# Kernel optimization log

Hardware: AMD Instinct MI355X
Metric: run time of the kernel (lower is better)

The kernel has to match this reference:

```python
import jax, jax.numpy as jnp
import numpy as np

EMBED_DIM = 1024
NUM_HEADS = 16
HEAD_DIM = EMBED_DIM // NUM_HEADS
B, S = 4, 2048


def setup_inputs() -> dict:
    key = jax.random.key(0)
    ks = jax.random.split(key, 9)
    scale = 1.0 / np.sqrt(EMBED_DIM)
    x = jax.random.normal(ks[0], (B, S, EMBED_DIM), dtype=jnp.float32)
    Wq = jax.random.normal(ks[1], (EMBED_DIM, EMBED_DIM), dtype=jnp.float32) * scale
    Wk = jax.random.normal(ks[2], (EMBED_DIM, EMBED_DIM), dtype=jnp.float32) * scale
    Wv = jax.random.normal(ks[3], (EMBED_DIM, EMBED_DIM), dtype=jnp.float32) * scale
    Wo = jax.random.normal(ks[4], (EMBED_DIM, EMBED_DIM), dtype=jnp.float32) * scale
    bq = jnp.zeros((EMBED_DIM,), jnp.float32)
    bk = jnp.zeros((EMBED_DIM,), jnp.float32)
    bv = jnp.zeros((EMBED_DIM,), jnp.float32)
    bo = jnp.zeros((EMBED_DIM,), jnp.float32)
    return {"x": x, "Wq": Wq, "bq": bq, "Wk": Wk, "bk": bk, "Wv": Wv, "bv": bv, "Wo": Wo, "bo": bo}


def _split_heads(t):
    # [B,S,E] -> [B,H,S,D]
    b, s, _ = t.shape
    return t.reshape(b, s, NUM_HEADS, HEAD_DIM).transpose(0, 2, 1, 3)


def reference(x, Wq, bq, Wk, bk, Wv, bv, Wo, bo):
    q = _split_heads(x @ Wq + bq)
    k = _split_heads(x @ Wk + bk)
    v = _split_heads(x @ Wv + bv)
    scale = 1.0 / jnp.sqrt(jnp.asarray(HEAD_DIM, x.dtype))
    scores = jnp.einsum('bhqd,bhkd->bhqk', q, k) * scale  # [B,H,S,S]
    weights = jax.nn.softmax(scores, axis=-1)
    attn = jnp.einsum('bhqk,bhkd->bhqd', weights, v)  # [B,H,S,D]
    b, h, s, d = attn.shape
    concat = attn.transpose(0, 2, 1, 3).reshape(b, s, h * d)
    return concat @ Wo + bo
```

## Files before the change

### kernel.cpp

```cpp
#include <hip/hip_runtime.h>
#include <hip/hip_bf16.h>

typedef unsigned short u16;
typedef __attribute__((ext_vector_type(8))) short bf16x8;
typedef __attribute__((ext_vector_type(4))) float f32x4;
typedef __attribute__((ext_vector_type(4))) unsigned short u16x4;

#define EMB 1024
#define SEQ 2048
#define NH 16
#define HD 64

#define OFF_WT   0u
#define OFF_WOT  3145728u
#define OFF_Q    4194304u
#define OFF_K    12582912u
#define OFF_VT   20971520u
#define OFF_OC   29360128u

#define QSCALE 0.1803368801111f

__device__ __forceinline__ u16 f2bf(float f) {
    unsigned int x; __builtin_memcpy(&x, &f, 4);
    unsigned int r = x + 0x7fffu + ((x >> 16) & 1u);
    return (u16)(r >> 16);
}

#if defined(__has_builtin) && __has_builtin(__builtin_amdgcn_cvt_pk_bf16_f32)
typedef __attribute__((ext_vector_type(2))) __bf16 bfv2;
__device__ __forceinline__ unsigned int pkbf(float a, float b) {
    bfv2 v = __builtin_amdgcn_cvt_pk_bf16_f32(a, b);
    unsigned int u; __builtin_memcpy(&u, &v, 4); return u;
}
#else
__device__ __forceinline__ unsigned int pkbf(float a, float b) {
    return (unsigned)f2bf(a) | ((unsigned)f2bf(b) << 16);
}
#endif

#if defined(__has_builtin) && __has_builtin(__builtin_amdgcn_exp2f)
__device__ __forceinline__ float exp2fast(float x) { return __builtin_amdgcn_exp2f(x); }
#else
__device__ __forceinline__ float exp2fast(float x) { return __builtin_exp2f(x); }
#endif

__device__ __forceinline__ void gld_lds16(const void* gsrc, void* ldst) {
    void* g = const_cast<void*>(gsrc);
    __builtin_amdgcn_global_load_lds((__attribute__((address_space(1))) void*)g,
                                     (__attribute__((address_space(3))) void*)ldst,
                                     16, 0, 0);
}

__global__ __launch_bounds__(256) void convert_x(
    const float* __restrict__ x, u16* __restrict__ xb)
{
    int i = (blockIdx.x * 256 + threadIdx.x) * 4;
    float4 v = *(const float4*)&x[i];
    uint2 o = { pkbf(v.x, v.y), pkbf(v.z, v.w) };
    *(uint2*)&xb[i] = o;
}

__global__ __launch_bounds__(256) void transpose_w(
    const float* __restrict__ W0, const float* __restrict__ W1,
    const float* __restrict__ W2, const float* __restrict__ W3,
    u16* __restrict__ ws)
{
    __shared__ u16 tile[64 * 65];
    const float* src = blockIdx.z == 0 ? W0 : blockIdx.z == 1 ? W1 : blockIdx.z == 2 ? W2 : W3;
    u16* dst = ws + (blockIdx.z < 3 ? (unsigned)blockIdx.z * 1048576u : OFF_WOT);
    const int k0 = blockIdx.x * 64, n0 = blockIdx.y * 64;
    const int t = threadIdx.x;
    #pragma unroll
    for (int i = 0; i < 16; i++) {
        int idx = i * 256 + t; int r = idx >> 6, c = idx & 63;
        tile[c * 65 + r] = f2bf(src[(k0 + r) * EMB + n0 + c]);
    }
    __syncthreads();
    #pragma unroll
    for (int i = 0; i < 16; i++) {
        int idx = i * 256 + t; int r = idx >> 6, c = idx & 63;
        dst[(n0 + r) * EMB + k0 + c] = tile[r * 65 + c];
    }
}

__global__ __launch_bounds__(256) void gemm_qkv(
    const u16* __restrict__ X, const u16* __restrict__ WT,
    const float* __restrict__ bq, const float* __restrict__ bk, const float* __restrict__ bv,
    u16* __restrict__ Qt, u16* __restrict__ Ko, u16* __restrict__ Vt)
{
    __shared__ u16 Al[128 * 32];
    __shared__ u16 Bl[128 * 32];
    const int t = threadIdx.x, lane = t & 63, w = t >> 6;
    const int quad = lane >> 4, l15 = lane & 15;
    const int wr = w >> 1, wc = w & 1;
    const int m0 = blockIdx.x * 128, n0 = blockIdx.y * 128;
    const f32x4 fzero = {0.f, 0.f, 0.f, 0.f};

    f32x4 acc[4][4];
    #pragma unroll
    for (int i = 0; i < 4; i++)
        #pragma unroll
        for (int j = 0; j < 4; j++) acc[i][j] = fzero;

    for (int kt = 0; kt < 32; ++kt) {
        #pragma unroll
        for (int r = 0; r < 2; r++) {
            int g = r * 256 + t; int row = g >> 2, cw = g & 3;
            int sc = (cw ^ ((row >> 1) & 3)) * 8;
            gld_lds16(X  + (size_t)(m0 + row) * EMB + kt * 32 + sc, &Al[g * 8]);
            gld_lds16(WT + (size_t)(n0 + row) * EMB + kt * 32 + sc, &Bl[g * 8]);
        }
        __syncthreads();
        bf16x8 af[4], bfr[4];
        #pragma unroll
        for (int i = 0; i < 4; i++) {
            int rowA = wr * 64 + i * 16 + l15;
            af[i] = *(const bf16x8*)&Al[rowA * 32 + ((quad ^ ((rowA >> 1) & 3)) * 8)];
        }
        #pragma unroll
        for (int j = 0; j < 4; j++) {
            int rowB = wc * 64 + j * 16 + l15;
            bfr[j] = *(const bf16x8*)&Bl[rowB * 32 + ((quad ^ ((rowB >> 1) & 3)) * 8)];
        }
        #pragma unroll
        for (int i = 0; i < 4; i++)
            #pragma unroll
            for (int j = 0; j < 4; j++)
                acc[i][j] = __builtin_amdgcn_mfma_f32_16x16x32_bf16(af[i], bfr[j], acc[i][j], 0, 0, 0);
        __syncthreads();
    }

    const int seg = n0 >> 10;
    const float* bias = seg == 0 ? bq : (seg == 1 ? bk : bv);
    #pragma unroll
    for (int j = 0; j < 4; j++) {
        int n = n0 + wc * 64 + j * 16 + l15;
        int nn = n & 1023;
        float bvl = bias[nn];
        int h = nn >> 6, d = nn & 63;
        #pragma unroll
        for (int i = 0; i < 4; i++) {
            int m = m0 + wr * 64 + i * 16 + quad * 4;
            int b = m >> 11, s = m & 2047;
            if (seg == 0) {
                uint2 pp = { pkbf((acc[i][j][0] + bvl) * QSCALE, (acc[i][j][1] + bvl) * QSCALE),
                             pkbf((acc[i][j][2] + bvl) * QSCALE, (acc[i][j][3] + bvl) * QSCALE) };
                *(uint2*)&Qt[(size_t)((b * NH + h) * HD + d) * SEQ + s] = pp;
            } else if (seg == 2) {
                uint2 pp = { pkbf(acc[i][j][0] + bvl, acc[i][j][1] + bvl),
                             pkbf(acc[i][j][2] + bvl, acc[i][j][3] + bvl) };
                *(uint2*)&Vt[(size_t)((b * NH + h) * HD + d) * SEQ + s] = pp;
            } else {
                size_t base = (size_t)((b * NH + h) * SEQ + s) * HD + d;
                #pragma unroll
                for (int r = 0; r < 4; r++) Ko[base + (size_t)r * HD] = f2bf(acc[i][j][r] + bvl);
            }
        }
    }
}

__global__ __launch_bounds__(256, 2) void flash_attn(
    const u16* __restrict__ Q, const u16* __restrict__ K,
    const u16* __restrict__ VT, u16* __restrict__ Oc)
{
    __shared__ u16 Kl[2][64 * 64];
    __shared__ u16 Vl[2][64 * 64];
    __shared__ u16 Pl[4][2][16 * 72];
    const int t = threadIdx.x, lane = t & 63, w = t >> 6;
    const int quad = lane >> 4, l15 = lane & 15;
    const int a7 = l15 & 7;
    const int bh = blockIdx.y;
    const int b = bh >> 4, h = bh & 15;
    const int q0 = blockIdx.x * 256 + w * 64;
    const u16* Qtb = Q + (size_t)bh * HD * SEQ;
    const u16* Kb  = K + (size_t)bh * SEQ * HD;
    const u16* Vb  = VT + (size_t)bh * HD * SEQ;
    const f32x4 fzero = {0.f, 0.f, 0.f, 0.f};

    const int kf0 = l15 * 64 + ((quad ^ a7) * 8);
    const int kf1 = l15 * 64 + (((4 + quad) ^ a7) * 8);
    u16* pww = &Pl[w][0][l15 * 72 + quad * 4];
    const u16* pwr = &Pl[w][0][l15 * 72 + quad * 8];

    bf16x8 ones;
    #pragma unroll
    for (int j = 0; j < 8; j++) ones[j] = (short)0x3F80;

    bf16x8 qf[4][2];
    #pragma unroll
    for (int i = 0; i < 4; i++)
        #pragma unroll
        for (int c = 0; c < 2; c++)
            #pragma unroll
            for (int j = 0; j < 8; j++)
                qf[i][c][j] = (short)Qtb[(size_t)(c * 32 + quad * 8 + j) * SEQ + q0 + i * 16 + l15];

    f32x4 oacc[4][4];
    f32x4 oextra[4];
    #pragma unroll
    for (int i = 0; i < 4; i++) {
        oextra[i] = fzero;
        #pragma unroll
        for (int f = 0; f < 4; f++) oacc[i][f] = fzero;
    }

    auto stage = [&](int kt, int bsel) {
        #pragma unroll
        for (int r = 0; r < 2; r++) {
            int g = r * 256 + t, row = g >> 3, cw = g & 7;
            int swz = (cw ^ (row & 7)) * 8;
            gld_lds16(Kb + (size_t)kt * 64 * HD + row * HD + swz, &Kl[bsel][g * 8]);
            gld_lds16(Vb + (size_t)row * SEQ + kt * 64 + swz, &Vl[bsel][g * 8]);
        }
    };

    stage(0, 0);
    asm volatile("s_waitcnt vmcnt(0) lgkmcnt(0)" ::: "memory");
    __builtin_amdgcn_s_barrier();
    __builtin_amdgcn_sched_barrier(0);

    int cur = 0;
    for (int kt = 0; kt < 32; ++kt) {
        if (kt < 31) stage(kt + 1, cur ^ 1);

        const u16* kbuf = &Kl[cur][0];
        const u16* vbuf = &Vl[cur][0];
        bf16x8 ak[2][4], av[2][4];
        #pragma unroll
        for (int f = 0; f < 4; f++) {
            ak[0][f] = *(const bf16x8*)(kbuf + kf0 + f * 1024);
            ak[1][f] = *(const bf16x8*)(kbuf + kf1 + f * 1024);
            av[0][f] = *(const bf16x8*)(vbuf + kf0 + f * 1024);
            av[1][f] = *(const bf16x8*)(vbuf + kf1 + f * 1024);
        }

        #pragma unroll
        for (int i = 0; i < 4; i++) {
            const int par = (i & 1) * 1152;
            f32x4 sf[4];
            #pragma unroll
            for (int f = 0; f < 4; f++) sf[f] = fzero;
            __builtin_amdgcn_s_setprio(1);
            #pragma unroll
            for (int c = 0; c < 2; c++)
                #pragma unroll
                for (int f = 0; f < 4; f++)
                    sf[f] = __builtin_amdgcn_mfma_f32_16x16x32_bf16(ak[c][f], qf[i][c], sf[f], 0, 0, 0);
            __builtin_amdgcn_s_setprio(0);

            #pragma unroll
            for (int f = 0; f < 4; f++) {
                float p0 = exp2fast(sf[f][0]);
                float p1 = exp2fast(sf[f][1]);
                float p2 = exp2fast(sf[f][2]);
                float p3 = exp2fast(sf[f][3]);
                uint2 pp = { pkbf(p0, p1), pkbf(p2, p3) };
                *(uint2*)(pww + par + f * 16) = pp;
            }
            bf16x8 bp0 = *(const bf16x8*)(pwr + par);
            bf16x8 bp1 = *(const bf16x8*)(pwr + par + 32);

            __builtin_amdgcn_s_setprio(1);
            #pragma unroll
            for (int f = 0; f < 4; f++) {
                oacc[i][f] = __builtin_amdgcn_mfma_f32_16x16x32_bf16(av[0][f], bp0, oacc[i][f], 0, 0, 0);
                oacc[i][f] = __builtin_amdgcn_mfma_f32_16x16x32_bf16(av[1][f], bp1, oacc[i][f], 0, 0, 0);
            }
            oextra[i] = __builtin_amdgcn_mfma_f32_16x16x32_bf16(ones, bp0, oextra[i], 0, 0, 0);
            oextra[i] = __builtin_amdgcn_mfma_f32_16x16x32_bf16(ones, bp1, oextra[i], 0, 0, 0);
            __builtin_amdgcn_s_setprio(0);
        }

        if (kt < 31) {
            asm volatile("s_waitcnt vmcnt(0) lgkmcnt(0)" ::: "memory");
            __builtin_amdgcn_s_barrier();
            __builtin_amdgcn_sched_barrier(0);
        }
        cur ^= 1;
    }

    #pragma unroll
    for (int i = 0; i < 4; i++) {
        float inv = 1.0f / oextra[i][0];
        int s = q0 + i * 16 + l15;
        size_t base = ((size_t)(b * SEQ + s) * NH + h) * HD;
        #pragma unroll
        for (int f = 0; f < 4; f++) {
            uint2 o = { pkbf(oacc[i][f][0] * inv, oacc[i][f][1] * inv),
                        pkbf(oacc[i][f][2] * inv, oacc[i][f][3] * inv) };
            *(uint2*)&Oc[base + f * 16 + quad * 4] = o;
        }
    }
}

__global__ __launch_bounds__(256) void gemm_out(
    const u16* __restrict__ A, const u16* __restrict__ WT,
    const float* __restrict__ bo, float* __restrict__ out)
{
    __shared__ u16 Al[128 * 32];
    __shared__ u16 Bl[128 * 32];
    const int t = threadIdx.x, lane = t & 63, w = t >> 6;
    const int quad = lane >> 4, l15 = lane & 15;
    const int wr = w >> 1, wc = w & 1;
    const int m0 = blockIdx.x * 128, n0 = blockIdx.y * 128;
    const f32x4 fzero = {0.f, 0.f, 0.f, 0.f};

    f32x4 acc[4][4];
    #pragma unroll
    for (int i = 0; i < 4; i++)
        #pragma unroll
        for (int j = 0; j < 4; j++) acc[i][j] = fzero;

    for (int kt = 0; kt < 32; ++kt) {
        #pragma unroll
        for (int r = 0; r < 2; r++) {
            int g = r * 256 + t; int row = g >> 2, cw = g & 3;
            int sc = (cw ^ ((row >> 1) & 3)) * 8;
            gld_lds16(A  + (size_t)(m0 + row) * EMB + kt * 32 + sc, &Al[g * 8]);
            gld_lds16(WT + (size_t)(n0 + row) * EMB + kt * 32 + sc, &Bl[g * 8]);
        }
        __syncthreads();
        bf16x8 af[4], bfr[4];
        #pragma unroll
        for (int i = 0; i < 4; i++) {
            int rowA = wr * 64 + i * 16 + l15;
            af[i] = *(const bf16x8*)&Al[rowA * 32 + ((quad ^ ((rowA >> 1) & 3)) * 8)];
        }
        #pragma unroll
        for (int j = 0; j < 4; j++) {
            int rowB = wc * 64 + j * 16 + l15;
            bfr[j] = *(const bf16x8*)&Bl[rowB * 32 + ((quad ^ ((rowB >> 1) & 3)) * 8)];
        }
        #pragma unroll
        for (int i = 0; i < 4; i++)
            #pragma unroll
            for (int j = 0; j < 4; j++)
                acc[i][j] = __builtin_amdgcn_mfma_f32_16x16x32_bf16(af[i], bfr[j], acc[i][j], 0, 0, 0);
        __syncthreads();
    }

    #pragma unroll
    for (int j = 0; j < 4; j++) {
        int n = n0 + wc * 64 + j * 16 + l15;
        float bvl = bo[n];
        #pragma unroll
        for (int i = 0; i < 4; i++) {
            int m = m0 + wr * 64 + i * 16 + quad * 4;
            #pragma unroll
            for (int r = 0; r < 4; r++)
                out[(size_t)(m + r) * EMB + n] = acc[i][j][r] + bvl;
        }
    }
}

extern "C" void kernel_launch(void* const* d_in, const int* in_sizes, int n_in,
                              void* d_out, int out_size, void* d_ws, size_t ws_size,
                              hipStream_t stream)
{
    (void)in_sizes; (void)n_in; (void)out_size; (void)ws_size;
    const float* x  = (const float*)d_in[0];
    const float* Wq = (const float*)d_in[1];
    const float* bq = (const float*)d_in[2];
    const float* Wk = (const float*)d_in[3];
    const float* bk = (const float*)d_in[4];
    const float* Wv = (const float*)d_in[5];
    const float* bv = (const float*)d_in[6];
    const float* Wo = (const float*)d_in[7];
    const float* bo = (const float*)d_in[8];
    u16* ws = (u16*)d_ws;
    u16* Xb = (u16*)d_out;

    convert_x<<<dim3(8192), 256, 0, stream>>>(x, Xb);
    transpose_w<<<dim3(16, 16, 4), 256, 0, stream>>>(Wq, Wk, Wv, Wo, ws);
    gemm_qkv<<<dim3(64, 24), 256, 0, stream>>>(Xb, ws + OFF_WT, bq, bk, bv,
                                               ws + OFF_Q, ws + OFF_K, ws + OFF_VT);
    flash_attn<<<dim3(8, 64), 256, 0, stream>>>(ws + OFF_Q, ws + OFF_K,
                                                ws + OFF_VT, ws + OFF_OC);
    gemm_out<<<dim3(64, 8), 256, 0, stream>>>(ws + OFF_OC, ws + OFF_WOT, bo, (float*)d_out);
}
```

Before: 295.9 us.

## Replace LDS round-trip for P with permlane swaps and remap blocks per XCD

The softmax probabilities P are no longer written to shared memory and read back in the B-operand layout. They are rearranged between lanes in registers using v_permlane32_swap and v_permlane16_swap, which removes the LDS traffic and the per-wave P buffer. Separately, the launch becomes a 1D grid that is remapped so that all query tiles of a given (batch, head) land on the same XCD, which should improve L2 reuse of K and V. The risk is that the permlane shuffle pattern must exactly reproduce the old LDS layout transform, or the results will be wrong.

```diff
diff --git a/kernel.cpp b/kernel.cpp
--- a/kernel.cpp
+++ b/kernel.cpp
@@ -4,7 +4,7 @@
 typedef unsigned short u16;
 typedef __attribute__((ext_vector_type(8))) short bf16x8;
 typedef __attribute__((ext_vector_type(4))) float f32x4;
-typedef __attribute__((ext_vector_type(4))) unsigned short u16x4;
+typedef __attribute__((ext_vector_type(4))) unsigned int u32x4;
 
 #define EMB 1024
 #define SEQ 2048
@@ -165,13 +165,17 @@
 {
     __shared__ u16 Kl[2][64 * 64];
     __shared__ u16 Vl[2][64 * 64];
-    __shared__ u16 Pl[4][2][16 * 72];
     const int t = threadIdx.x, lane = t & 63, w = t >> 6;
     const int quad = lane >> 4, l15 = lane & 15;
     const int a7 = l15 & 7;
-    const int bh = blockIdx.y;
+
+    const int lin = blockIdx.x;
+    const int xcd = lin & 7, slot = lin >> 3;
+    const int bh = xcd * 8 + (slot >> 3);
+    const int qx = slot & 7;
     const int b = bh >> 4, h = bh & 15;
-    const int q0 = blockIdx.x * 256 + w * 64;
+    const int q0 = qx * 256 + w * 64;
+
     const u16* Qtb = Q + (size_t)bh * HD * SEQ;
     const u16* Kb  = K + (size_t)bh * SEQ * HD;
     const u16* Vb  = VT + (size_t)bh * HD * SEQ;
@@ -179,8 +183,6 @@
 
     const int kf0 = l15 * 64 + ((quad ^ a7) * 8);
     const int kf1 = l15 * 64 + (((4 + quad) ^ a7) * 8);
-    u16* pww = &Pl[w][0][l15 * 72 + quad * 4];
-    const u16* pwr = &Pl[w][0][l15 * 72 + quad * 8];
 
     bf16x8 ones;
     #pragma unroll
@@ -236,7 +238,6 @@
 
         #pragma unroll
         for (int i = 0; i < 4; i++) {
-            const int par = (i & 1) * 1152;
             f32x4 sf[4];
             #pragma unroll
             for (int f = 0; f < 4; f++) sf[f] = fzero;
@@ -248,17 +249,29 @@
                     sf[f] = __builtin_amdgcn_mfma_f32_16x16x32_bf16(ak[c][f], qf[i][c], sf[f], 0, 0, 0);
             __builtin_amdgcn_s_setprio(0);
 
+            unsigned int pa[4][2];
             #pragma unroll
             for (int f = 0; f < 4; f++) {
-                float p0 = exp2fast(sf[f][0]);
-                float p1 = exp2fast(sf[f][1]);
-                float p2 = exp2fast(sf[f][2]);
-                float p3 = exp2fast(sf[f][3]);
-                uint2 pp = { pkbf(p0, p1), pkbf(p2, p3) };
-                *(uint2*)(pww + par + f * 16) = pp;
+                pa[f][0] = pkbf(exp2fast(sf[f][0]), exp2fast(sf[f][1]));
+                pa[f][1] = pkbf(exp2fast(sf[f][2]), exp2fast(sf[f][3]));
             }
-            bf16x8 bp0 = *(const bf16x8*)(pwr + par);
-            bf16x8 bp1 = *(const bf16x8*)(pwr + par + 32);
+
+            unsigned int z0 = pa[0][0], w0 = pa[1][0];
+            asm("v_permlane32_swap_b32 %0, %1" : "+v"(z0), "+v"(w0));
+            asm("v_permlane16_swap_b32 %0, %1" : "+v"(z0), "+v"(w0));
+            unsigned int z1 = pa[0][1], w1 = pa[1][1];
+            asm("v_permlane32_swap_b32 %0, %1" : "+v"(z1), "+v"(w1));
+            asm("v_permlane16_swap_b32 %0, %1" : "+v"(z1), "+v"(w1));
+            unsigned int z2 = pa[2][0], w2 = pa[3][0];
+            asm("v_permlane32_swap_b32 %0, %1" : "+v"(z2), "+v"(w2));
+            asm("v_permlane16_swap_b32 %0, %1" : "+v"(z2), "+v"(w2));
+            unsigned int z3 = pa[2][1], w3 = pa[3][1];
+            asm("v_permlane32_swap_b32 %0, %1" : "+v"(z3), "+v"(w3));
+            asm("v_permlane16_swap_b32 %0, %1" : "+v"(z3), "+v"(w3));
+
+            bf16x8 bp0, bp1;
+            { u32x4 u = {z0, z1, w0, w1}; __builtin_memcpy(&bp0, &u, 16); }
+            { u32x4 u = {z2, z3, w2, w3}; __builtin_memcpy(&bp1, &u, 16); }
 
             __builtin_amdgcn_s_setprio(1);
             #pragma unroll
@@ -374,7 +387,7 @@
     transpose_w<<<dim3(16, 16, 4), 256, 0, stream>>>(Wq, Wk, Wv, Wo, ws);
     gemm_qkv<<<dim3(64, 24), 256, 0, stream>>>(Xb, ws + OFF_WT, bq, bk, bv,
                                                ws + OFF_Q, ws + OFF_K, ws + OFF_VT);
-    flash_attn<<<dim3(8, 64), 256, 0, stream>>>(ws + OFF_Q, ws + OFF_K,
-                                                ws + OFF_VT, ws + OFF_OC);
+    flash_attn<<<dim3(512), 256, 0, stream>>>(ws + OFF_Q, ws + OFF_K,
+                                              ws + OFF_VT, ws + OFF_OC);
     gemm_out<<<dim3(64, 8), 256, 0, stream>>>(ws + OFF_OC, ws + OFF_WOT, bo, (float*)d_out);
 }
```

New measurement: 293.4 us. No clear change (-0.8%).
